# Kernel optimization log

Hardware: AMD Instinct MI355X
Metric: run time of the kernel (lower is better)

Reference implementation:

```python
import jax, jax.numpy as jnp
import numpy as np

N_NODES = 150000
N_EDGES = 2400000


def gcn_conv(x, W, b, src, dst, n):
    """PyG GCNConv: add self-loops, symmetric D^-1/2 A_hat D^-1/2 norm, x@W then scatter-sum, + bias."""
    h = x @ W  # [N, out]
    loop = jnp.arange(n)
    s = jnp.concatenate([src, loop])
    d = jnp.concatenate([dst, loop])
    deg = jax.ops.segment_sum(jnp.ones(s.shape, dtype=h.dtype), d, num_segments=n)
    dis = jnp.where(deg > 0, jax.lax.rsqrt(jnp.maximum(deg, 1e-12)), 0.0)
    norm = dis[s] * dis[d]  # [E+N]
    out = jax.ops.segment_sum(h[s] * norm[:, None], d, num_segments=n)
    return out + b


def setup_inputs() -> dict:
    key = jax.random.key(0)
    ks = jax.random.split(key, 16)
    d = 32
    inp = {
        "x": jax.random.normal(ks[0], (N_NODES, 2), dtype=jnp.float32),
        "edge_index": jax.random.randint(ks[1], (2, N_EDGES), 0, N_NODES, dtype=jnp.int64),
        "fc1_w": jax.random.normal(ks[2], (2, d), dtype=jnp.float32) * 0.5,
        "fc1_b": jax.random.normal(ks[3], (d,), dtype=jnp.float32) * 0.1,
        "conv1_w": jax.random.normal(ks[4], (d, d), dtype=jnp.float32) * (1.0 / np.sqrt(d)),
        "conv1_b": jax.random.normal(ks[5], (d,), dtype=jnp.float32) * 0.1,
        "conv2_w": jax.random.normal(ks[6], (d, d), dtype=jnp.float32) * (1.0 / np.sqrt(d)),
        "conv2_b": jax.random.normal(ks[7], (d,), dtype=jnp.float32) * 0.1,
        "conv31_w": jax.random.normal(ks[8], (d, d), dtype=jnp.float32) * (1.0 / np.sqrt(d)),
        "conv31_b": jax.random.normal(ks[9], (d,), dtype=jnp.float32) * 0.1,
        "conv32_w": jax.random.normal(ks[10], (d, d), dtype=jnp.float32) * (1.0 / np.sqrt(d)),
        "conv32_b": jax.random.normal(ks[11], (d,), dtype=jnp.float32) * 0.1,
        "fc21_w": jax.random.normal(ks[12], (d, 1), dtype=jnp.float32) * (1.0 / np.sqrt(d)),
        "fc21_b": jax.random.normal(ks[13], (1,), dtype=jnp.float32) * 0.1,
        "fc22_w": jax.random.normal(ks[14], (d, 1), dtype=jnp.float32) * (1.0 / np.sqrt(d)),
        "fc22_b": jax.random.normal(ks[15], (1,), dtype=jnp.float32) * 0.1,
    }
    return inp


def reference(x, edge_index, fc1_w, fc1_b, conv1_w, conv1_b, conv2_w, conv2_b,
              conv31_w, conv31_b, conv32_w, conv32_b, fc21_w, fc21_b, fc22_w, fc22_b):
    n = x.shape[0]
    src, dst = edge_index[0], edge_index[1]
    h = jax.nn.relu(x @ fc1_w + fc1_b)
    h = jax.nn.relu(gcn_conv(h, conv1_w, conv1_b, src, dst, n))
    h = jax.nn.relu(gcn_conv(h, conv2_w, conv2_b, src, dst, n))
    x1 = jax.nn.relu(gcn_conv(h, conv31_w, conv31_b, src, dst, n)) @ fc21_w + fc21_b
    x2 = jax.nn.relu(gcn_conv(h, conv32_w, conv32_b, src, dst, n)) @ fc22_w + fc22_b
    return jnp.concatenate([x1, x2], axis=1)  # [N, 2]
```

## Files before the change

### kernel.cpp

```cpp
#include <hip/hip_runtime.h>

#define N_NODES 150000
#define N_EDGES 2400000
#define D 32
#define NBUCK 1172
#define CHUNK 4096
#define NCHK 586
#define CSR_CAP (N_EDGES + 3 * N_NODES + 64)

__global__ void k_zero_row(float* __restrict__ HA, float* __restrict__ HB) {
    int t = threadIdx.x;
    HA[(size_t)N_NODES * D + t] = 0.f;
    HB[(size_t)N_NODES * D + t] = 0.f;
}

__global__ __launch_bounds__(256) void kA_hist(const int* __restrict__ dst,
                                               int* __restrict__ cnt) {
    __shared__ int bins[NBUCK];
    int t = threadIdx.x;
    for (int k = t; k < NBUCK; k += 256) bins[k] = 0;
    __syncthreads();
    int e0 = blockIdx.x * CHUNK;
#pragma unroll
    for (int r = 0; r < CHUNK / 256; ++r) {
        int e = e0 + r * 256 + t;
        if (e < N_EDGES) atomicAdd(&bins[dst[e] >> 7], 1);
    }
    __syncthreads();
    for (int k = t; k < NBUCK; k += 256) cnt[blockIdx.x * NBUCK + k] = bins[k];
}

__global__ __launch_bounds__(256) void kS1(int* __restrict__ cnt, int* __restrict__ bstart) {
    __shared__ int tile[8][33];
    __shared__ int carry[32];
    int t = threadIdx.x;
    int tl = t & 31, tr = t >> 5;
    int b = blockIdx.x * 32 + tl;
    if (t < 32) carry[t] = 0;
    __syncthreads();
    for (int c0 = 0; c0 < NCHK; c0 += 8) {
        int c = c0 + tr;
        int v = (c < NCHK && b < NBUCK) ? cnt[c * NBUCK + b] : 0;
        tile[tr][tl] = v;
        __syncthreads();
        if (t < 32) {
            int s = carry[t];
#pragma unroll
            for (int r = 0; r < 8; ++r) { int x = tile[r][t]; tile[r][t] = s; s += x; }
            carry[t] = s;
        }
        __syncthreads();
        if (c < NCHK && b < NBUCK) cnt[c * NBUCK + b] = tile[tr][tl];
        __syncthreads();
    }
    if (t < 32 && b < NBUCK) bstart[b] = carry[t];
}

__global__ void k_scan_small(int* __restrict__ a, int m) {
    __shared__ int s[256];
    __shared__ int carry;
    int t = threadIdx.x;
    if (t == 0) carry = 0;
    __syncthreads();
    for (int base = 0; base < m; base += 256) {
        int v = (base + t < m) ? a[base + t] : 0;
        s[t] = v;
        __syncthreads();
        for (int off = 1; off < 256; off <<= 1) {
            int add = (t >= off) ? s[t - off] : 0;
            __syncthreads();
            s[t] += add;
            __syncthreads();
        }
        int c0 = carry;
        if (base + t < m) a[base + t] = c0 + s[t] - v;
        int bsum = s[255];
        __syncthreads();
        if (t == 0) carry = c0 + bsum;
        __syncthreads();
    }
    if (t == 0) a[m] = carry;
}

__global__ __launch_bounds__(256) void kB_scatter(const int* __restrict__ src,
                                                  const int* __restrict__ dst,
                                                  const int* __restrict__ cnt,
                                                  const int* __restrict__ bstart,
                                                  int* __restrict__ ebuf) {
    __shared__ int lofs[NBUCK];
    int t = threadIdx.x;
    for (int k = t; k < NBUCK; k += 256)
        lofs[k] = bstart[k] + cnt[blockIdx.x * NBUCK + k];
    __syncthreads();
    int e0 = blockIdx.x * CHUNK;
#pragma unroll
    for (int r = 0; r < CHUNK / 256; ++r) {
        int e = e0 + r * 256 + t;
        if (e < N_EDGES) {
            int d = dst[e];
            int p = atomicAdd(&lofs[d >> 7], 1);
            ebuf[p] = src[e] | ((d & 127) << 18);
        }
    }
}

__global__ __launch_bounds__(256) void kC1(const int* __restrict__ ebuf,
                                           const int* __restrict__ bstart,
                                           const float2* __restrict__ x,
                                           int* __restrict__ deg,
                                           float* __restrict__ dis,
                                           float4* __restrict__ xd,
                                           int* __restrict__ pbase) {
    __shared__ int hist[128];
    __shared__ int sc[128];
    int b = blockIdx.x, t = threadIdx.x;
    if (t < 128) hist[t] = 0;
    __syncthreads();
    int s0 = bstart[b], s1 = bstart[b + 1];
    for (int e = s0 + t; e < s1; e += 256) atomicAdd(&hist[ebuf[e] >> 18], 1);
    __syncthreads();
    int i = b * 128 + t;
    if (t < 128) {
        int dv = hist[t];
        if (i < N_NODES) {
            deg[i] = dv;
            float dz = rsqrtf((float)dv + 1.0f);
            dis[i] = dz;
            float2 xv = x[i];
            xd[i] = make_float4(xv.x, xv.y, dz, 0.f);
        } else if (i == N_NODES) {
            xd[i] = make_float4(0.f, 0.f, 0.f, 0.f);
        }
        sc[t] = (i < N_NODES) ? ((dv + 3) & ~3) : 0;
    }
    __syncthreads();
    for (int s = 64; s > 0; s >>= 1) {
        if (t < s) sc[t] += sc[t + s];
        __syncthreads();
    }
    if (t == 0) pbase[b] = sc[0];
}

__global__ __launch_bounds__(256) void kC3(const int* __restrict__ ebuf,
                                           const int* __restrict__ bstart,
                                           const int* __restrict__ deg,
                                           const int* __restrict__ pbase,
                                           int* __restrict__ csr,
                                           int* __restrict__ irow) {
    __shared__ int sc[128];
    __shared__ int loff[128];
    __shared__ int pos[128];
    int b = blockIdx.x, t = threadIdx.x;
    if (b == 0) {
        if (t == 0) irow[N_NODES] = pbase[NBUCK];
        if (t < 64) csr[pbase[NBUCK] + t] = N_NODES;
    }
    int i = b * 128 + t;
    int dv = 0, pad = 0;
    if (t < 128) {
        dv = (i < N_NODES) ? deg[i] : 0;
        pad = (dv + 3) & ~3;
        sc[t] = pad;
        pos[t] = 0;
    }
    __syncthreads();
    for (int off = 1; off < 128; off <<= 1) {
        int add = 0;
        if (t < 128 && t >= off) add = sc[t - off];
        __syncthreads();
        if (t < 128) sc[t] += add;
        __syncthreads();
    }
    int base = pbase[b];
    if (t < 128) {
        loff[t] = sc[t] - pad;
        if (i < N_NODES) irow[i] = base + loff[t];
    }
    __syncthreads();
    int s0 = bstart[b], s1 = bstart[b + 1];
    for (int e = s0 + t; e < s1; e += 256) {
        int v = ebuf[e];
        int dl = v >> 18;
        int p = atomicAdd(&pos[dl], 1);
        csr[base + loff[dl] + p] = v & 0x3FFFF;
    }
    __syncthreads();
    if (t < 128 && i < N_NODES) {
        int st = base + loff[t] + dv, en = base + loff[t] + pad;
        for (int q = st; q < en; ++q) csr[q] = N_NODES;
    }
}

__global__ __launch_bounds__(256) void k_layer1f(const float4* __restrict__ xd,
                                                 const int* __restrict__ row,
                                                 const int* __restrict__ csr,
                                                 const float* __restrict__ W,
                                                 const float* __restrict__ bf,
                                                 const float* __restrict__ Wc,
                                                 const float* __restrict__ bc,
                                                 float* __restrict__ hout) {
    __shared__ float4 stage[8][16];
    __shared__ float arow[8][32];
    int g = threadIdx.x >> 5, l = threadIdx.x & 31, f = l;
    int t = blockIdx.x * 256 + threadIdx.x;
    int i = t >> 5;
    if (i >= N_NODES) return;
    float w0 = W[f], w1 = W[D + f], bb = bf[f];
    float wcol[D];
#pragma unroll
    for (int k = 0; k < D; ++k) wcol[k] = Wc[k * D + f];
    float4 sv = xd[i];
    float hs = fmaf(sv.x, w0, fmaf(sv.y, w1, bb));
    hs = hs > 0.f ? hs : 0.f;
    float a = hs * sv.z;
    int rs = row[i], re = row[i + 1];
    int j0 = rs;
    int cs = csr[j0 + (l & 15)];
    while (j0 < re) {
        int nxt = csr[j0 + 16 + (l & 15)];
        if (l < 16) {
            int s2 = (j0 + l < re) ? cs : N_NODES;
            stage[g][l] = xd[s2];
        }
#pragma unroll
        for (int it = 0; it < 4; ++it) {
            if (j0 + it * 4 >= re) break;
            float4 v0 = stage[g][it * 4 + 0];
            float4 v1 = stage[g][it * 4 + 1];
            float4 v2 = stage[g][it * 4 + 2];
            float4 v3 = stage[g][it * 4 + 3];
            float h0 = fmaf(v0.x, w0, fmaf(v0.y, w1, bb)); h0 = h0 > 0.f ? h0 : 0.f;
            float h1 = fmaf(v1.x, w0, fmaf(v1.y, w1, bb)); h1 = h1 > 0.f ? h1 : 0.f;
            float h2 = fmaf(v2.x, w0, fmaf(v2.y, w1, bb)); h2 = h2 > 0.f ? h2 : 0.f;
            float h3 = fmaf(v3.x, w0, fmaf(v3.y, w1, bb)); h3 = h3 > 0.f ? h3 : 0.f;
            a = fmaf(h0, v0.z, a);
            a = fmaf(h1, v1.z, a);
            a = fmaf(h2, v2.z, a);
            a = fmaf(h3, v3.z, a);
        }
        cs = nxt;
        j0 += 16;
    }
    float di = sv.z;
    a *= di;
    arow[g][f] = a;
    float acc = 0.f;
#pragma unroll
    for (int q = 0; q < 8; ++q) {
        float4 aq = ((const float4*)arow[g])[q];
        acc = fmaf(aq.x, wcol[4 * q + 0],
              fmaf(aq.y, wcol[4 * q + 1],
              fmaf(aq.z, wcol[4 * q + 2],
              fmaf(aq.w, wcol[4 * q + 3], acc))));
    }
    float v = acc + bc[f];
    v = v > 0.f ? v : 0.f;
    hout[t] = v * di;
}

__global__ __launch_bounds__(256) void k_layer(const float* __restrict__ hsc,
                                               const int* __restrict__ row,
                                               const int* __restrict__ csr,
                                               const float* __restrict__ dis,
                                               const float* __restrict__ W,
                                               const float* __restrict__ b,
                                               float* __restrict__ hout) {
    __shared__ float arow[8][32];
    int g = threadIdx.x >> 5, l = threadIdx.x & 31, f = l;
    int t = blockIdx.x * 256 + threadIdx.x;
    int i = t >> 5;
    if (i >= N_NODES) return;
    float wcol[D];
#pragma unroll
    for (int k = 0; k < D; ++k) wcol[k] = W[k * D + f];
    int c = l & 7;
    const float4* rowf4 = (const float4*)hsc;
    float4 a4 = make_float4(0.f, 0.f, 0.f, 0.f);
    int rs = row[i], re = row[i + 1];
    int j0 = rs;
    int sidx = csr[j0 + (l & 15)];
    while (j0 < re) {
        int nxt = csr[j0 + 16 + (l & 15)];
#pragma unroll
        for (int it = 0; it < 4; ++it) {
            if (j0 + it * 4 >= re) break;
            int s = __shfl(sidx, it * 4 + (l >> 3), 32);
            float4 v = rowf4[s * 8 + c];
            a4.x += v.x; a4.y += v.y; a4.z += v.z; a4.w += v.w;
        }
        sidx = nxt;
        j0 += 16;
    }
    a4.x += __shfl_xor(a4.x, 8, 32);  a4.y += __shfl_xor(a4.y, 8, 32);
    a4.z += __shfl_xor(a4.z, 8, 32);  a4.w += __shfl_xor(a4.w, 8, 32);
    a4.x += __shfl_xor(a4.x, 16, 32); a4.y += __shfl_xor(a4.y, 16, 32);
    a4.z += __shfl_xor(a4.z, 16, 32); a4.w += __shfl_xor(a4.w, 16, 32);
    float4 sv = rowf4[i * 8 + c];
    a4.x += sv.x; a4.y += sv.y; a4.z += sv.z; a4.w += sv.w;
    float di = dis[i];
    a4.x *= di; a4.y *= di; a4.z *= di; a4.w *= di;
    if (l < 8) ((float4*)arow[g])[l] = a4;
    float acc = 0.f;
#pragma unroll
    for (int q = 0; q < 8; ++q) {
        float4 aq = ((const float4*)arow[g])[q];
        acc = fmaf(aq.x, wcol[4 * q + 0],
              fmaf(aq.y, wcol[4 * q + 1],
              fmaf(aq.z, wcol[4 * q + 2],
              fmaf(aq.w, wcol[4 * q + 3], acc))));
    }
    float v = acc + b[f];
    v = v > 0.f ? v : 0.f;
    hout[t] = v * di;
}

__global__ __launch_bounds__(256) void k_heads(
    const float* __restrict__ hsc, const int* __restrict__ row,
    const int* __restrict__ csr, const float* __restrict__ dis,
    const float* __restrict__ W1, const float* __restrict__ b1,
    const float* __restrict__ W2, const float* __restrict__ b2,
    const float* __restrict__ fw1, const float* __restrict__ fb1,
    const float* __restrict__ fw2, const float* __restrict__ fb2,
    float* __restrict__ out) {
    __shared__ float arow[8][32];
    int g = threadIdx.x >> 5, l = threadIdx.x & 31, f = l;
    int t = blockIdx.x * 256 + threadIdx.x;
    int i = t >> 5;
    if (i >= N_NODES) return;
    float wc1[D], wc2[D];
#pragma unroll
    for (int k = 0; k < D; ++k) { wc1[k] = W1[k * D + f]; wc2[k] = W2[k * D + f]; }
    int c = l & 7;
    const float4* rowf4 = (const float4*)hsc;
    float4 a4 = make_float4(0.f, 0.f, 0.f, 0.f);
    int rs = row[i], re = row[i + 1];
    int j0 = rs;
    int sidx = csr[j0 + (l & 15)];
    while (j0 < re) {
        int nxt = csr[j0 + 16 + (l & 15)];
#pragma unroll
        for (int it = 0; it < 4; ++it) {
            if (j0 + it * 4 >= re) break;
            int s = __shfl(sidx, it * 4 + (l >> 3), 32);
            float4 v = rowf4[s * 8 + c];
            a4.x += v.x; a4.y += v.y; a4.z += v.z; a4.w += v.w;
        }
        sidx = nxt;
        j0 += 16;
    }
    a4.x += __shfl_xor(a4.x, 8, 32);  a4.y += __shfl_xor(a4.y, 8, 32);
    a4.z += __shfl_xor(a4.z, 8, 32);  a4.w += __shfl_xor(a4.w, 8, 32);
    a4.x += __shfl_xor(a4.x, 16, 32); a4.y += __shfl_xor(a4.y, 16, 32);
    a4.z += __shfl_xor(a4.z, 16, 32); a4.w += __shfl_xor(a4.w, 16, 32);
    float4 sv = rowf4[i * 8 + c];
    a4.x += sv.x; a4.y += sv.y; a4.z += sv.z; a4.w += sv.w;
    float di = dis[i];
    a4.x *= di; a4.y *= di; a4.z *= di; a4.w *= di;
    if (l < 8) ((float4*)arow[g])[l] = a4;
    float acc1 = 0.f, acc2 = 0.f;
#pragma unroll
    for (int q = 0; q < 8; ++q) {
        float4 aq = ((const float4*)arow[g])[q];
        acc1 = fmaf(aq.x, wc1[4 * q + 0],
               fmaf(aq.y, wc1[4 * q + 1],
               fmaf(aq.z, wc1[4 * q + 2],
               fmaf(aq.w, wc1[4 * q + 3], acc1))));
        acc2 = fmaf(aq.x, wc2[4 * q + 0],
               fmaf(aq.y, wc2[4 * q + 1],
               fmaf(aq.z, wc2[4 * q + 2],
               fmaf(aq.w, wc2[4 * q + 3], acc2))));
    }
    float v1 = acc1 + b1[f];
    v1 = (v1 > 0.f ? v1 : 0.f) * fw1[f];
    float v2 = acc2 + b2[f];
    v2 = (v2 > 0.f ? v2 : 0.f) * fw2[f];
#pragma unroll
    for (int o = 16; o > 0; o >>= 1) {
        v1 += __shfl_down(v1, o, 32);
        v2 += __shfl_down(v2, o, 32);
    }
    if (f == 0) {
        out[i * 2] = v1 + fb1[0];
        out[i * 2 + 1] = v2 + fb2[0];
    }
}

extern "C" void kernel_launch(void* const* d_in, const int* in_sizes, int n_in,
                              void* d_out, int out_size, void* d_ws, size_t ws_size,
                              hipStream_t stream) {
    const float* x       = (const float*)d_in[0];
    const int*   eidx    = (const int*)d_in[1];
    const float* fc1_w   = (const float*)d_in[2];
    const float* fc1_b   = (const float*)d_in[3];
    const float* conv1_w = (const float*)d_in[4];
    const float* conv1_b = (const float*)d_in[5];
    const float* conv2_w = (const float*)d_in[6];
    const float* conv2_b = (const float*)d_in[7];
    const float* c31_w   = (const float*)d_in[8];
    const float* c31_b   = (const float*)d_in[9];
    const float* c32_w   = (const float*)d_in[10];
    const float* c32_b   = (const float*)d_in[11];
    const float* fc21_w  = (const float*)d_in[12];
    const float* fc21_b  = (const float*)d_in[13];
    const float* fc22_w  = (const float*)d_in[14];
    const float* fc22_b  = (const float*)d_in[15];
    float* out = (float*)d_out;

    const int* src = eidx;
    const int* dst = eidx + N_EDGES;

    int*   wsb    = (int*)d_ws;
    int*   csr    = wsb;
    int*   irow   = wsb + 2850064;
    int*   bstart = wsb + 3000068;
    int*   pbase  = wsb + 3001242;
    float* dis    = (float*)(wsb + 3002416);
    float* HA     = (float*)(wsb + 3152416);
    float* HB     = (float*)(wsb + 7952448);
    int*    cnt  = (int*)HA;
    int*    ebuf = (int*)HA + 700000;
    float4* xd   = (float4*)((int*)HA + 3100016);
    int*    deg  = (int*)HB;

    const int BLK = 256;
    const int gL  = (N_NODES * D + BLK - 1) / BLK;

    k_zero_row<<<1, 32, 0, stream>>>(HA, HB);
    kA_hist<<<NCHK, BLK, 0, stream>>>(dst, cnt);
    kS1<<<(NBUCK + 31) / 32, BLK, 0, stream>>>(cnt, bstart);
    k_scan_small<<<1, BLK, 0, stream>>>(bstart, NBUCK);
    kB_scatter<<<NCHK, BLK, 0, stream>>>(src, dst, cnt, bstart, ebuf);
    kC1<<<NBUCK, BLK, 0, stream>>>(ebuf, bstart, (const float2*)x, deg, dis, xd, pbase);
    k_scan_small<<<1, BLK, 0, stream>>>(pbase, NBUCK);
    kC3<<<NBUCK, BLK, 0, stream>>>(ebuf, bstart, deg, pbase, csr, irow);

    k_layer1f<<<gL, BLK, 0, stream>>>(xd, irow, csr, fc1_w, fc1_b, conv1_w, conv1_b, HB);
    k_layer<<<gL, BLK, 0, stream>>>(HB, irow, csr, dis, conv2_w, conv2_b, HA);
    k_heads<<<gL, BLK, 0, stream>>>(HA, irow, csr, dis, c31_w, c31_b, c32_w, c32_b,
                                    fc21_w, fc21_b, fc22_w, fc22_b, out);
}
```

Before: 302.6 us.

## Process two nodes per 32-lane group in layer and head kernels

Each 32-lane group in k_layer and k_heads now handles two consecutive nodes, interleaving their neighbor gathers so more independent loads are in flight and the weight columns loaded into registers are reused across two nodes. The grid shrinks by half accordingly. The separate zero-row kernel is folded into kC3 to drop one launch. Register pressure rises from the duplicated gather buffers, which may lower occupancy, and load imbalance between the paired nodes adds tail loops.

```diff
diff --git a/kernel.cpp b/kernel.cpp
--- a/kernel.cpp
+++ b/kernel.cpp
@@ -7,12 +7,6 @@
 #define CHUNK 4096
 #define NCHK 586
 #define CSR_CAP (N_EDGES + 3 * N_NODES + 64)
-
-__global__ void k_zero_row(float* __restrict__ HA, float* __restrict__ HB) {
-    int t = threadIdx.x;
-    HA[(size_t)N_NODES * D + t] = 0.f;
-    HB[(size_t)N_NODES * D + t] = 0.f;
-}
 
 __global__ __launch_bounds__(256) void kA_hist(const int* __restrict__ dst,
                                                int* __restrict__ cnt) {
@@ -146,7 +140,9 @@
                                            const int* __restrict__ deg,
                                            const int* __restrict__ pbase,
                                            int* __restrict__ csr,
-                                           int* __restrict__ irow) {
+                                           int* __restrict__ irow,
+                                           float* __restrict__ HA,
+                                           float* __restrict__ HB) {
     __shared__ int sc[128];
     __shared__ int loff[128];
     __shared__ int pos[128];
@@ -154,6 +150,8 @@
     if (b == 0) {
         if (t == 0) irow[N_NODES] = pbase[NBUCK];
         if (t < 64) csr[pbase[NBUCK] + t] = N_NODES;
+        if (t >= 64 && t < 96) HA[(size_t)N_NODES * D + (t - 64)] = 0.f;
+        if (t >= 96 && t < 128) HB[(size_t)N_NODES * D + (t - 96)] = 0.f;
     }
     int i = b * 128 + t;
     int dv = 0, pad = 0;
@@ -265,53 +263,92 @@
                                                const float* __restrict__ W,
                                                const float* __restrict__ b,
                                                float* __restrict__ hout) {
-    __shared__ float arow[8][32];
+    __shared__ float arow[16][32];
     int g = threadIdx.x >> 5, l = threadIdx.x & 31, f = l;
-    int t = blockIdx.x * 256 + threadIdx.x;
-    int i = t >> 5;
-    if (i >= N_NODES) return;
+    int gg = blockIdx.x * 8 + g;
+    int iA = gg * 2, iB = iA + 1;
     float wcol[D];
 #pragma unroll
     for (int k = 0; k < D; ++k) wcol[k] = W[k * D + f];
-    int c = l & 7;
+    int c = l & 7, l16 = l & 15, sub = l >> 3;
     const float4* rowf4 = (const float4*)hsc;
-    float4 a4 = make_float4(0.f, 0.f, 0.f, 0.f);
-    int rs = row[i], re = row[i + 1];
-    int j0 = rs;
-    int sidx = csr[j0 + (l & 15)];
-    while (j0 < re) {
-        int nxt = csr[j0 + 16 + (l & 15)];
+    int rsA = row[iA], mid = row[iB], reB = row[iB + 1];
+    float4 aA = make_float4(0.f, 0.f, 0.f, 0.f);
+    float4 aB = make_float4(0.f, 0.f, 0.f, 0.f);
+    int jA = rsA, jB = mid;
+    int csA = csr[jA + l16], csB = csr[jB + l16];
+    while (jA < mid && jB < reB) {
+        int nA = csr[jA + 16 + l16], nB = csr[jB + 16 + l16];
+        float4 vA[4], vB[4];
+#pragma unroll
+        for (int it = 0; it < 4; ++it)
+            if (jA + it * 4 < mid) { int s = __shfl(csA, it * 4 + sub, 32); vA[it] = rowf4[s * 8 + c]; }
+#pragma unroll
+        for (int it = 0; it < 4; ++it)
+            if (jB + it * 4 < reB) { int s = __shfl(csB, it * 4 + sub, 32); vB[it] = rowf4[s * 8 + c]; }
 #pragma unroll
         for (int it = 0; it < 4; ++it) {
-            if (j0 + it * 4 >= re) break;
-            int s = __shfl(sidx, it * 4 + (l >> 3), 32);
-            float4 v = rowf4[s * 8 + c];
-            a4.x += v.x; a4.y += v.y; a4.z += v.z; a4.w += v.w;
-        }
-        sidx = nxt;
-        j0 += 16;
-    }
-    a4.x += __shfl_xor(a4.x, 8, 32);  a4.y += __shfl_xor(a4.y, 8, 32);
-    a4.z += __shfl_xor(a4.z, 8, 32);  a4.w += __shfl_xor(a4.w, 8, 32);
-    a4.x += __shfl_xor(a4.x, 16, 32); a4.y += __shfl_xor(a4.y, 16, 32);
-    a4.z += __shfl_xor(a4.z, 16, 32); a4.w += __shfl_xor(a4.w, 16, 32);
-    float4 sv = rowf4[i * 8 + c];
-    a4.x += sv.x; a4.y += sv.y; a4.z += sv.z; a4.w += sv.w;
-    float di = dis[i];
-    a4.x *= di; a4.y *= di; a4.z *= di; a4.w *= di;
-    if (l < 8) ((float4*)arow[g])[l] = a4;
-    float acc = 0.f;
+            if (jA + it * 4 < mid) { aA.x += vA[it].x; aA.y += vA[it].y; aA.z += vA[it].z; aA.w += vA[it].w; }
+            if (jB + it * 4 < reB) { aB.x += vB[it].x; aB.y += vB[it].y; aB.z += vB[it].z; aB.w += vB[it].w; }
+        }
+        csA = nA; csB = nB; jA += 16; jB += 16;
+    }
+    while (jA < mid) {
+        int nA = csr[jA + 16 + l16];
+        float4 vA[4];
+#pragma unroll
+        for (int it = 0; it < 4; ++it)
+            if (jA + it * 4 < mid) { int s = __shfl(csA, it * 4 + sub, 32); vA[it] = rowf4[s * 8 + c]; }
+#pragma unroll
+        for (int it = 0; it < 4; ++it)
+            if (jA + it * 4 < mid) { aA.x += vA[it].x; aA.y += vA[it].y; aA.z += vA[it].z; aA.w += vA[it].w; }
+        csA = nA; jA += 16;
+    }
+    while (jB < reB) {
+        int nB = csr[jB + 16 + l16];
+        float4 vB[4];
+#pragma unroll
+        for (int it = 0; it < 4; ++it)
+            if (jB + it * 4 < reB) { int s = __shfl(csB, it * 4 + sub, 32); vB[it] = rowf4[s * 8 + c]; }
+#pragma unroll
+        for (int it = 0; it < 4; ++it)
+            if (jB + it * 4 < reB) { aB.x += vB[it].x; aB.y += vB[it].y; aB.z += vB[it].z; aB.w += vB[it].w; }
+        csB = nB; jB += 16;
+    }
+    aA.x += __shfl_xor(aA.x, 8, 32);  aA.y += __shfl_xor(aA.y, 8, 32);
+    aA.z += __shfl_xor(aA.z, 8, 32);  aA.w += __shfl_xor(aA.w, 8, 32);
+    aA.x += __shfl_xor(aA.x, 16, 32); aA.y += __shfl_xor(aA.y, 16, 32);
+    aA.z += __shfl_xor(aA.z, 16, 32); aA.w += __shfl_xor(aA.w, 16, 32);
+    aB.x += __shfl_xor(aB.x, 8, 32);  aB.y += __shfl_xor(aB.y, 8, 32);
+    aB.z += __shfl_xor(aB.z, 8, 32);  aB.w += __shfl_xor(aB.w, 8, 32);
+    aB.x += __shfl_xor(aB.x, 16, 32); aB.y += __shfl_xor(aB.y, 16, 32);
+    aB.z += __shfl_xor(aB.z, 16, 32); aB.w += __shfl_xor(aB.w, 16, 32);
+    float4 svA = rowf4[iA * 8 + c], svB = rowf4[iB * 8 + c];
+    float diA = dis[iA], diB = dis[iB];
+    aA.x = (aA.x + svA.x) * diA; aA.y = (aA.y + svA.y) * diA;
+    aA.z = (aA.z + svA.z) * diA; aA.w = (aA.w + svA.w) * diA;
+    aB.x = (aB.x + svB.x) * diB; aB.y = (aB.y + svB.y) * diB;
+    aB.z = (aB.z + svB.z) * diB; aB.w = (aB.w + svB.w) * diB;
+    if (l < 8) ((float4*)arow[g * 2])[l] = aA;
+    else if (l < 16) ((float4*)arow[g * 2 + 1])[l - 8] = aB;
+    float accA = 0.f, accB = 0.f;
 #pragma unroll
     for (int q = 0; q < 8; ++q) {
-        float4 aq = ((const float4*)arow[g])[q];
-        acc = fmaf(aq.x, wcol[4 * q + 0],
-              fmaf(aq.y, wcol[4 * q + 1],
-              fmaf(aq.z, wcol[4 * q + 2],
-              fmaf(aq.w, wcol[4 * q + 3], acc))));
-    }
-    float v = acc + b[f];
-    v = v > 0.f ? v : 0.f;
-    hout[t] = v * di;
+        float4 qa = ((const float4*)arow[g * 2])[q];
+        float4 qb = ((const float4*)arow[g * 2 + 1])[q];
+        accA = fmaf(qa.x, wcol[4 * q + 0],
+               fmaf(qa.y, wcol[4 * q + 1],
+               fmaf(qa.z, wcol[4 * q + 2],
+               fmaf(qa.w, wcol[4 * q + 3], accA))));
+        accB = fmaf(qb.x, wcol[4 * q + 0],
+               fmaf(qb.y, wcol[4 * q + 1],
+               fmaf(qb.z, wcol[4 * q + 2],
+               fmaf(qb.w, wcol[4 * q + 3], accB))));
+    }
+    float vA_ = accA + b[f]; vA_ = vA_ > 0.f ? vA_ : 0.f;
+    float vB_ = accB + b[f]; vB_ = vB_ > 0.f ? vB_ : 0.f;
+    hout[iA * D + f] = vA_ * diA;
+    hout[iB * D + f] = vB_ * diB;
 }
 
 __global__ __launch_bounds__(256) void k_heads(
@@ -322,66 +359,102 @@
     const float* __restrict__ fw1, const float* __restrict__ fb1,
     const float* __restrict__ fw2, const float* __restrict__ fb2,
     float* __restrict__ out) {
-    __shared__ float arow[8][32];
+    __shared__ float arow[16][32];
     int g = threadIdx.x >> 5, l = threadIdx.x & 31, f = l;
-    int t = blockIdx.x * 256 + threadIdx.x;
-    int i = t >> 5;
-    if (i >= N_NODES) return;
+    int gg = blockIdx.x * 8 + g;
+    int iA = gg * 2, iB = iA + 1;
     float wc1[D], wc2[D];
 #pragma unroll
     for (int k = 0; k < D; ++k) { wc1[k] = W1[k * D + f]; wc2[k] = W2[k * D + f]; }
-    int c = l & 7;
+    int c = l & 7, l16 = l & 15, sub = l >> 3;
     const float4* rowf4 = (const float4*)hsc;
-    float4 a4 = make_float4(0.f, 0.f, 0.f, 0.f);
-    int rs = row[i], re = row[i + 1];
-    int j0 = rs;
-    int sidx = csr[j0 + (l & 15)];
-    while (j0 < re) {
-        int nxt = csr[j0 + 16 + (l & 15)];
+    int rsA = row[iA], mid = row[iB], reB = row[iB + 1];
+    float4 aA = make_float4(0.f, 0.f, 0.f, 0.f);
+    float4 aB = make_float4(0.f, 0.f, 0.f, 0.f);
+    int jA = rsA, jB = mid;
+    int csA = csr[jA + l16], csB = csr[jB + l16];
+    while (jA < mid && jB < reB) {
+        int nA = csr[jA + 16 + l16], nB = csr[jB + 16 + l16];
+        float4 vA[4], vB[4];
+#pragma unroll
+        for (int it = 0; it < 4; ++it)
+            if (jA + it * 4 < mid) { int s = __shfl(csA, it * 4 + sub, 32); vA[it] = rowf4[s * 8 + c]; }
+#pragma unroll
+        for (int it = 0; it < 4; ++it)
+            if (jB + it * 4 < reB) { int s = __shfl(csB, it * 4 + sub, 32); vB[it] = rowf4[s * 8 + c]; }
 #pragma unroll
         for (int it = 0; it < 4; ++it) {
-            if (j0 + it * 4 >= re) break;
-            int s = __shfl(sidx, it * 4 + (l >> 3), 32);
-            float4 v = rowf4[s * 8 + c];
-            a4.x += v.x; a4.y += v.y; a4.z += v.z; a4.w += v.w;
-        }
-        sidx = nxt;
-        j0 += 16;
-    }
-    a4.x += __shfl_xor(a4.x, 8, 32);  a4.y += __shfl_xor(a4.y, 8, 32);
-    a4.z += __shfl_xor(a4.z, 8, 32);  a4.w += __shfl_xor(a4.w, 8, 32);
-    a4.x += __shfl_xor(a4.x, 16, 32); a4.y += __shfl_xor(a4.y, 16, 32);
-    a4.z += __shfl_xor(a4.z, 16, 32); a4.w += __shfl_xor(a4.w, 16, 32);
-    float4 sv = rowf4[i * 8 + c];
-    a4.x += sv.x; a4.y += sv.y; a4.z += sv.z; a4.w += sv.w;
-    float di = dis[i];
-    a4.x *= di; a4.y *= di; a4.z *= di; a4.w *= di;
-    if (l < 8) ((float4*)arow[g])[l] = a4;
-    float acc1 = 0.f, acc2 = 0.f;
+            if (jA + it * 4 < mid) { aA.x += vA[it].x; aA.y += vA[it].y; aA.z += vA[it].z; aA.w += vA[it].w; }
+            if (jB + it * 4 < reB) { aB.x += vB[it].x; aB.y += vB[it].y; aB.z += vB[it].z; aB.w += vB[it].w; }
+        }
+        csA = nA; csB = nB; jA += 16; jB += 16;
+    }
+    while (jA < mid) {
+        int nA = csr[jA + 16 + l16];
+        float4 vA[4];
+#pragma unroll
+        for (int it = 0; it < 4; ++it)
+            if (jA + it * 4 < mid) { int s = __shfl(csA, it * 4 + sub, 32); vA[it] = rowf4[s * 8 + c]; }
+#pragma unroll
+        for (int it = 0; it < 4; ++it)
+            if (jA + it * 4 < mid) { aA.x += vA[it].x; aA.y += vA[it].y; aA.z += vA[it].z; aA.w += vA[it].w; }
+        csA = nA; jA += 16;
+    }
+    while (jB < reB) {
+        int nB = csr[jB + 16 + l16];
+        float4 vB[4];
+#pragma unroll
+        for (int it = 0; it < 4; ++it)
+            if (jB + it * 4 < reB) { int s = __shfl(csB, it * 4 + sub, 32); vB[it] = rowf4[s * 8 + c]; }
+#pragma unroll
+        for (int it = 0; it < 4; ++it)
+            if (jB + it * 4 < reB) { aB.x += vB[it].x; aB.y += vB[it].y; aB.z += vB[it].z; aB.w += vB[it].w; }
+        csB = nB; jB += 16;
+    }
+    aA.x += __shfl_xor(aA.x, 8, 32);  aA.y += __shfl_xor(aA.y, 8, 32);
+    aA.z += __shfl_xor(aA.z, 8, 32);  aA.w += __shfl_xor(aA.w, 8, 32);
+    aA.x += __shfl_xor(aA.x, 16, 32); aA.y += __shfl_xor(aA.y, 16, 32);
+    aA.z += __shfl_xor(aA.z, 16, 32); aA.w += __shfl_xor(aA.w, 16, 32);
+    aB.x += __shfl_xor(aB.x, 8, 32);  aB.y += __shfl_xor(aB.y, 8, 32);
+    aB.z += __shfl_xor(aB.z, 8, 32);  aB.w += __shfl_xor(aB.w, 8, 32);
+    aB.x += __shfl_xor(aB.x, 16, 32); aB.y += __shfl_xor(aB.y, 16, 32);
+    aB.z += __shfl_xor(aB.z, 16, 32); aB.w += __shfl_xor(aB.w, 16, 32);
+    float4 svA = rowf4[iA * 8 + c], svB = rowf4[iB * 8 + c];
+    float diA = dis[iA], diB = dis[iB];
+    aA.x = (aA.x + svA.x) * diA; aA.y = (aA.y + svA.y) * diA;
+    aA.z = (aA.z + svA.z) * diA; aA.w = (aA.w + svA.w) * diA;
+    aB.x = (aB.x + svB.x) * diB; aB.y = (aB.y + svB.y) * diB;
+    aB.z = (aB.z + svB.z) * diB; aB.w = (aB.w + svB.w) * diB;
+    if (l < 8) ((float4*)arow[g * 2])[l] = aA;
+    else if (l < 16) ((float4*)arow[g * 2 + 1])[l - 8] = aB;
+    float a1A = 0.f, a2A = 0.f, a1B = 0.f, a2B = 0.f;
 #pragma unroll
     for (int q = 0; q < 8; ++q) {
-        float4 aq = ((const float4*)arow[g])[q];
-        acc1 = fmaf(aq.x, wc1[4 * q + 0],
-               fmaf(aq.y, wc1[4 * q + 1],
-               fmaf(aq.z, wc1[4 * q + 2],
-               fmaf(aq.w, wc1[4 * q + 3], acc1))));
-        acc2 = fmaf(aq.x, wc2[4 * q + 0],
-               fmaf(aq.y, wc2[4 * q + 1],
-               fmaf(aq.z, wc2[4 * q + 2],
-               fmaf(aq.w, wc2[4 * q + 3], acc2))));
-    }
-    float v1 = acc1 + b1[f];
-    v1 = (v1 > 0.f ? v1 : 0.f) * fw1[f];
-    float v2 = acc2 + b2[f];
-    v2 = (v2 > 0.f ? v2 : 0.f) * fw2[f];
+        float4 qa = ((const float4*)arow[g * 2])[q];
+        float4 qb = ((const float4*)arow[g * 2 + 1])[q];
+        a1A = fmaf(qa.x, wc1[4 * q + 0], fmaf(qa.y, wc1[4 * q + 1],
+              fmaf(qa.z, wc1[4 * q + 2], fmaf(qa.w, wc1[4 * q + 3], a1A))));
+        a2A = fmaf(qa.x, wc2[4 * q + 0], fmaf(qa.y, wc2[4 * q + 1],
+              fmaf(qa.z, wc2[4 * q + 2], fmaf(qa.w, wc2[4 * q + 3], a2A))));
+        a1B = fmaf(qb.x, wc1[4 * q + 0], fmaf(qb.y, wc1[4 * q + 1],
+              fmaf(qb.z, wc1[4 * q + 2], fmaf(qb.w, wc1[4 * q + 3], a1B))));
+        a2B = fmaf(qb.x, wc2[4 * q + 0], fmaf(qb.y, wc2[4 * q + 1],
+              fmaf(qb.z, wc2[4 * q + 2], fmaf(qb.w, wc2[4 * q + 3], a2B))));
+    }
+    float v1A = a1A + b1[f]; v1A = (v1A > 0.f ? v1A : 0.f) * fw1[f];
+    float v2A = a2A + b2[f]; v2A = (v2A > 0.f ? v2A : 0.f) * fw2[f];
+    float v1B = a1B + b1[f]; v1B = (v1B > 0.f ? v1B : 0.f) * fw1[f];
+    float v2B = a2B + b2[f]; v2B = (v2B > 0.f ? v2B : 0.f) * fw2[f];
 #pragma unroll
     for (int o = 16; o > 0; o >>= 1) {
-        v1 += __shfl_down(v1, o, 32);
-        v2 += __shfl_down(v2, o, 32);
-    }
-    if (f == 0) {
-        out[i * 2] = v1 + fb1[0];
-        out[i * 2 + 1] = v2 + fb2[0];
+        v1A += __shfl_down(v1A, o, 32);
+        v2A += __shfl_down(v2A, o, 32);
+        v1B += __shfl_down(v1B, o, 32);
+        v2B += __shfl_down(v2B, o, 32);
+    }
+    if (l == 0) {
+        float4 o4 = make_float4(v1A + fb1[0], v2A + fb2[0], v1B + fb1[0], v2B + fb2[0]);
+        *(float4*)&out[iA * 2] = o4;
     }
 }
 
@@ -424,18 +497,18 @@
 
     const int BLK = 256;
     const int gL  = (N_NODES * D + BLK - 1) / BLK;
-
-    k_zero_row<<<1, 32, 0, stream>>>(HA, HB);
+    const int gL2 = N_NODES / 16;
+
     kA_hist<<<NCHK, BLK, 0, stream>>>(dst, cnt);
     kS1<<<(NBUCK + 31) / 32, BLK, 0, stream>>>(cnt, bstart);
     k_scan_small<<<1, BLK, 0, stream>>>(bstart, NBUCK);
     kB_scatter<<<NCHK, BLK, 0, stream>>>(src, dst, cnt, bstart, ebuf);
     kC1<<<NBUCK, BLK, 0, stream>>>(ebuf, bstart, (const float2*)x, deg, dis, xd, pbase);
     k_scan_small<<<1, BLK, 0, stream>>>(pbase, NBUCK);
-    kC3<<<NBUCK, BLK, 0, stream>>>(ebuf, bstart, deg, pbase, csr, irow);
+    kC3<<<NBUCK, BLK, 0, stream>>>(ebuf, bstart, deg, pbase, csr, irow, HA, HB);
 
     k_layer1f<<<gL, BLK, 0, stream>>>(xd, irow, csr, fc1_w, fc1_b, conv1_w, conv1_b, HB);
-    k_layer<<<gL, BLK, 0, stream>>>(HB, irow, csr, dis, conv2_w, conv2_b, HA);
-    k_heads<<<gL, BLK, 0, stream>>>(HA, irow, csr, dis, c31_w, c31_b, c32_w, c32_b,
-                                    fc21_w, fc21_b, fc22_w, fc22_b, out);
-}
+    k_layer<<<gL2, BLK, 0, stream>>>(HB, irow, csr, dis, conv2_w, conv2_b, HA);
+    k_heads<<<gL2, BLK, 0, stream>>>(HA, irow, csr, dis, c31_w, c31_b, c32_w, c32_b,
+                                     fc21_w, fc21_b, fc22_w, fc22_b, out);
+}
```

Result: faster. 257.6 us (-14.9%).
